# Performance work log

Hardware: AMD Instinct MI355X
Metric: run time of the kernel (lower is better)

## Reference

```python
import jax, jax.numpy as jnp
import numpy as np

B, S, C, H, W = 8, 32, 3, 256, 256


def setup_inputs() -> dict:
    key = jax.random.key(0)
    k1, k2 = jax.random.split(key)
    return {
        "input": jax.random.normal(k1, (B, S, C, H, W), dtype=jnp.float32),
        "target": jax.random.normal(k2, (B, C, H, W), dtype=jnp.float32),
    }


def _l2norm(x, axis):
    # F.normalize: x / max(||x||_2, eps)
    return x / jnp.maximum(jnp.linalg.norm(x, axis=axis, keepdims=True), 1e-12)


def _forward(input, target):
    b, s, c, h, w = input.shape
    # target: [B,C,H,W] -> permute(0,1,3,2) -> [B,C,W,H] -> flatten(1,2) -> [B, C*W, H]
    target_f = _l2norm(jnp.transpose(target, (0, 1, 3, 2)).reshape(b, c * w, h), axis=1)
    # input: [B,S,C,H,W] -> permute(0,1,2,4,3) -> [B,S,C,W,H] -> flatten(2,3) -> [B,S,C*W,H]
    input_f = _l2norm(jnp.transpose(input, (0, 1, 2, 4, 3)).reshape(b, s, c * w, h), axis=2)

    def corr_one(xf, wf):
        # xf: [S, C*W, H] as conv batch, wf: [C*W, H] as single-output-channel kernel
        y = jax.lax.conv_general_dilated(
            xf, wf[None], window_strides=(1,), padding=[(h - 1, h - 1)],
            dimension_numbers=("NCH", "OIH", "NCH"))
        return y[:, 0, :h]  # first H shift positions (overlap sizes 1..H)

    corr = jax.vmap(corr_one)(input_f, target_f)  # [B, S, H]
    corr = corr / jnp.arange(1, h + 1, dtype=input.dtype)  # mean over overlap size

    overlap = jnp.argmax(corr, axis=-1)            # [B, S] best overlap per sample
    shift = (h - 1) - overlap                      # rows to shift up by

    # out[b,s,:,r,:] = input[b,s,:,r+shift,:] for r < overlap, else 0
    h_idx = jnp.arange(h)[None, None, :] + shift[:, :, None]  # [B, S, H]
    valid = h_idx < h
    idx = jnp.clip(h_idx, 0, h - 1)[:, :, None, :, None]      # [B,S,1,H,1]
    gathered = jnp.take_along_axis(input, idx, axis=3)
    return jnp.where(valid[:, :, None, :, None], gathered, jnp.zeros((), input.dtype))


def reference(input, target):
    return _forward(input, target)
```

## Files before the change

### kernel.cpp

```cpp
#include <hip/hip_runtime.h>

#define B_ 8
#define S_ 32
#define C_ 3
#define H_ 256
#define W_ 256
#define HW_ (H_*W_)
#define CHW_ (C_*H_*W_)

typedef __attribute__((ext_vector_type(8))) short bf16x8;
typedef __attribute__((ext_vector_type(4))) float f32x4;

__device__ __forceinline__ void split2(float x, float y, unsigned &hp, unsigned &lp) {
  unsigned ux = __float_as_uint(x), uy = __float_as_uint(y);
  unsigned hx = ux & 0xFFFF0000u, hy = uy & 0xFFFF0000u;
  float lx = x - __uint_as_float(hx);
  float ly = y - __uint_as_float(hy);
  hp = (ux >> 16) | hy;
  lp = (__float_as_uint(lx) >> 16) | (__float_as_uint(ly) & 0xFFFF0000u);
}

__global__ __launch_bounds__(512)
void ct_corr_mfma(const float* __restrict__ input,
                  const float* __restrict__ target,
                  int* __restrict__ shift_out) {
  __shared__ ushort Ah[2][8192], Al[2][8192], Bh[2][8192], Bl[2][8192];
  __shared__ float ninSq[256], ntgSq[256], rnin[256], rntg[256], corrS[256];
  __shared__ unsigned long long wkey[4];

  const int bs = blockIdx.x;
  const int b  = bs >> 5;
  const int t  = threadIdx.x;
  const int lane = t & 63;
  const int wid  = t >> 6;
  const int wm   = wid >> 2;
  const int wn   = wid & 3;

  const float* Abase = input  + (size_t)bs * CHW_;
  const float* Tbase = target + (size_t)b  * CHW_;

  if (t < 256) { ninSq[t] = 0.f; ntgSq[t] = 0.f; corrS[t] = 0.f; }

  f32x4 acc[8][4];
#pragma unroll
  for (int m = 0; m < 8; ++m)
#pragma unroll
    for (int n = 0; n < 4; ++n) acc[m][n] = (f32x4){0.f, 0.f, 0.f, 0.f};

  float4 pa[4], pb[4];
  float ssA[4] = {0.f, 0.f, 0.f, 0.f};
  float ssB[4] = {0.f, 0.f, 0.f, 0.f};

  auto issue = [&](int kt) {
    const float* Ab = Abase + (size_t)(kt >> 3) * HW_ + (kt & 7) * 32;
    const float* Tb = Tbase + (size_t)(kt >> 3) * HW_ + (kt & 7) * 32;
#pragma unroll
    for (int p = 0; p < 4; ++p) {
      int f   = p * 512 + t;
      int row = (f >> 7) * 16 + ((f >> 1) & 15);
      int kk  = ((f >> 5) & 3) * 8 + (f & 1) * 4;
      pa[p] = *(const float4*)(Ab + (size_t)row * W_ + kk);
      pb[p] = *(const float4*)(Tb + (size_t)row * W_ + kk);
    }
  };

  auto stash = [&](int sel) {
    ushort* AhD = Ah[sel]; ushort* AlD = Al[sel];
    ushort* BhD = Bh[sel]; ushort* BlD = Bl[sel];
#pragma unroll
    for (int p = 0; p < 4; ++p) {
      int f   = p * 512 + t;
      int idx = (f >> 7) * 512 + ((f >> 5) & 3) * 128 + ((f >> 1) & 15) * 8 + (f & 1) * 4;
      float4 va = pa[p], vb = pb[p];
      ssA[p] = fmaf(va.x, va.x, fmaf(va.y, va.y, fmaf(va.z, va.z, fmaf(va.w, va.w, ssA[p]))));
      ssB[p] = fmaf(vb.x, vb.x, fmaf(vb.y, vb.y, fmaf(vb.z, vb.z, fmaf(vb.w, vb.w, ssB[p]))));
      unsigned h0, l0, h1, l1;
      split2(va.x, va.y, h0, l0); split2(va.z, va.w, h1, l1);
      *(uint2*)&AhD[idx] = make_uint2(h0, h1);
      *(uint2*)&AlD[idx] = make_uint2(l0, l1);
      split2(vb.x, vb.y, h0, l0); split2(vb.z, vb.w, h1, l1);
      *(uint2*)&BhD[idx] = make_uint2(h0, h1);
      *(uint2*)&BlD[idx] = make_uint2(l0, l1);
    }
  };

  issue(0);
  stash(0);
  issue(1);
  __syncthreads();

  for (int kt = 0; kt < 24; ++kt) {
    const int cur = kt & 1, nx = cur ^ 1;
    const ushort* AhC = Ah[cur]; const ushort* AlC = Al[cur];
    const ushort* BhC = Bh[cur]; const ushort* BlC = Bl[cur];

    bf16x8 bh[4], bl[4];
#pragma unroll
    for (int n = 0; n < 4; ++n) {
      int ct = wn * 4 + n;
      bh[n] = *(const bf16x8*)&BhC[ct * 512 + lane * 8];
      bl[n] = *(const bf16x8*)&BlC[ct * 512 + lane * 8];
    }
#pragma unroll
    for (int m = 0; m < 8; ++m) {
      int rt = wm * 8 + m;
      bf16x8 ah = *(const bf16x8*)&AhC[rt * 512 + lane * 8];
      bf16x8 al = *(const bf16x8*)&AlC[rt * 512 + lane * 8];
#pragma unroll
      for (int n = 0; n < 4; ++n) {
        acc[m][n] = __builtin_amdgcn_mfma_f32_16x16x32_bf16(ah, bh[n], acc[m][n], 0, 0, 0);
        acc[m][n] = __builtin_amdgcn_mfma_f32_16x16x32_bf16(ah, bl[n], acc[m][n], 0, 0, 0);
        acc[m][n] = __builtin_amdgcn_mfma_f32_16x16x32_bf16(al, bh[n], acc[m][n], 0, 0, 0);
      }
    }
    if (kt < 23) stash(nx);
    if (kt < 22) issue(kt + 2);
    __syncthreads();
  }

#pragma unroll
  for (int p = 0; p < 4; ++p) {
    int row = (p * 4 + (t >> 7)) * 16 + ((t >> 1) & 15);
    atomicAdd(&ninSq[row], ssA[p]);
    atomicAdd(&ntgSq[row], ssB[p]);
  }
  __syncthreads();
  if (t < 256) {
    rnin[t] = 1.0f / fmaxf(sqrtf(ninSq[t]), 1e-12f);
    rntg[t] = 1.0f / fmaxf(sqrtf(ntgSq[t]), 1e-12f);
  }
  __syncthreads();

#pragma unroll
  for (int n = 0; n < 4; ++n) {
    int col = wn * 64 + n * 16 + (lane & 15);
    float rc = rntg[col];
#pragma unroll
    for (int m = 0; m < 8; ++m) {
      f32x4 a = acc[m][n];
#pragma unroll
      for (int r = 0; r < 4; ++r) {
        int row = wm * 128 + m * 16 + (lane >> 4) * 4 + r;
        int q = col - row;
        if (q >= 0) atomicAdd(&corrS[q], a[r] * rnin[row] * rc);
      }
    }
  }
  __syncthreads();

  if (t < 256) {
    int q = 255 - t;
    float v = corrS[q] / (float)(256 - q);
    unsigned u = __float_as_uint(v);
    u = (u & 0x80000000u) ? ~u : (u | 0x80000000u);
    unsigned long long key = ((unsigned long long)u << 32) | (unsigned)q;
#pragma unroll
    for (int off = 32; off; off >>= 1) {
      unsigned long long o = __shfl_xor(key, off);
      if (o > key) key = o;
    }
    if ((t & 63) == 0) wkey[t >> 6] = key;
  }
  __syncthreads();
  if (t == 0) {
    unsigned long long k = wkey[0];
#pragma unroll
    for (int i = 1; i < 4; ++i) if (wkey[i] > k) k = wkey[i];
    shift_out[bs] = (int)(k & 0xFFFFFFFFull);
  }
}

__global__ void ct_gather(const float* __restrict__ input,
                          const int* __restrict__ shift,
                          float* __restrict__ out) {
  size_t idx = (size_t)blockIdx.x * blockDim.x + threadIdx.x;
  int w4 = (int)(idx & 63);
  int h  = (int)((idx >> 6) & 255);
  int sc = (int)(idx >> 14);
  int bs = sc / 3;
  int hh = h + shift[bs];
  float4 v = make_float4(0.f, 0.f, 0.f, 0.f);
  if (hh < H_) v = *(const float4*)(input + ((size_t)sc << 16) + (size_t)hh * W_ + w4*4);
  *(float4*)(out + (idx << 2)) = v;
}

extern "C" void kernel_launch(void* const* d_in, const int* in_sizes, int n_in,
                              void* d_out, int out_size, void* d_ws, size_t ws_size,
                              hipStream_t stream) {
  const float* input  = (const float*)d_in[0];
  const float* target = (const float*)d_in[1];
  float* out  = (float*)d_out;
  int*  shift = (int*)d_ws;

  ct_corr_mfma <<<B_ * S_, 512, 0, stream>>>(input, target, shift);
  ct_gather    <<<(B_*S_*C_*H_*W_/4) / 256, 256, 0, stream>>>(input, shift, out);
}
```

Measured before the change: 167.4 us.

## Pre-split target into bf16 hi/lo tiles and stream via direct global-to-LDS loads

```diff
diff --git a/kernel.cpp b/kernel.cpp
--- a/kernel.cpp
+++ b/kernel.cpp
@@ -7,9 +7,14 @@
 #define W_ 256
 #define HW_ (H_*W_)
 #define CHW_ (C_*H_*W_)
+#define NT_ 24
+#define TILE_ELEMS 8192
 
 typedef __attribute__((ext_vector_type(8))) short bf16x8;
 typedef __attribute__((ext_vector_type(4))) float f32x4;
+typedef unsigned int u32;
+typedef u32 __attribute__((address_space(3)))* lds_u32p;
+typedef const u32 __attribute__((address_space(1)))* glb_u32p;
 
 __device__ __forceinline__ void split2(float x, float y, unsigned &hp, unsigned &lp) {
   unsigned ux = __float_as_uint(x), uy = __float_as_uint(y);
@@ -20,26 +25,70 @@
   lp = (__float_as_uint(lx) >> 16) | (__float_as_uint(ly) & 0xFFFF0000u);
 }
 
+__device__ __forceinline__ void gl2lds16(const ushort* g, ushort* l) {
+  __builtin_amdgcn_global_load_lds((glb_u32p)g, (lds_u32p)l, 16, 0, 0);
+}
+
+__global__ void ct_ntg(const float* __restrict__ target, float* __restrict__ rntg) {
+  int r = (int)((blockIdx.x * (size_t)blockDim.x + threadIdx.x) >> 6);
+  int lane = threadIdx.x & 63;
+  const float* base = target + (size_t)(r >> 8) * CHW_ + (size_t)(r & 255) * W_;
+  float ss = 0.f;
+#pragma unroll
+  for (int c = 0; c < C_; ++c)
+#pragma unroll
+    for (int tt = 0; tt < W_/64; ++tt) {
+      float v = base[c*HW_ + tt*64 + lane];
+      ss = fmaf(v, v, ss);
+    }
+#pragma unroll
+  for (int off = 32; off; off >>= 1) ss += __shfl_xor(ss, off);
+  if (lane == 0) rntg[r] = 1.0f / fmaxf(sqrtf(ss), 1e-12f);
+}
+
+__global__ void ct_bsplit(const float* __restrict__ target,
+                          ushort* __restrict__ BhG, ushort* __restrict__ BlG) {
+  int bx = blockIdx.x;
+  int b  = bx / 24, kt = bx % 24;
+  int c  = kt >> 3, w0 = (kt & 7) * 32;
+  int t  = threadIdx.x;
+  int trow = t >> 3, tw = t & 7;
+  const float* base = target + (size_t)(b*C_ + c) * HW_ + w0 + tw*4;
+  ushort* oh = BhG + (size_t)bx * TILE_ELEMS;
+  ushort* ol = BlG + (size_t)bx * TILE_ELEMS;
+#pragma unroll
+  for (int i = 0; i < 8; ++i) {
+    int row = trow + 32*i;
+    float4 v = *(const float4*)(base + (size_t)row * W_);
+    unsigned h0, l0, h1, l1;
+    split2(v.x, v.y, h0, l0); split2(v.z, v.w, h1, l1);
+    int idx = (row>>4)*512 + (tw>>1)*128 + (row&15)*8 + (tw&1)*4;
+    *(uint2*)&oh[idx] = make_uint2(h0, h1);
+    *(uint2*)&ol[idx] = make_uint2(l0, l1);
+  }
+}
+
 __global__ __launch_bounds__(512)
 void ct_corr_mfma(const float* __restrict__ input,
-                  const float* __restrict__ target,
+                  const ushort* __restrict__ BhG, const ushort* __restrict__ BlG,
+                  const float* __restrict__ rntg_g,
                   int* __restrict__ shift_out) {
-  __shared__ ushort Ah[2][8192], Al[2][8192], Bh[2][8192], Bl[2][8192];
-  __shared__ float ninSq[256], ntgSq[256], rnin[256], rntg[256], corrS[256];
+  __shared__ ushort AhL[2][TILE_ELEMS], AlL[2][TILE_ELEMS];
+  __shared__ ushort BhL[2][TILE_ELEMS], BlL[2][TILE_ELEMS];
+  __shared__ float ninSq[256], rnin[256], rntg_s[256], corrS[256];
   __shared__ unsigned long long wkey[4];
 
   const int bs = blockIdx.x;
-  const int b  = bs >> 5;
+  const int bG = bs >> 5;
   const int t  = threadIdx.x;
   const int lane = t & 63;
   const int wid  = t >> 6;
   const int wm   = wid >> 2;
   const int wn   = wid & 3;
 
-  const float* Abase = input  + (size_t)bs * CHW_;
-  const float* Tbase = target + (size_t)b  * CHW_;
-
-  if (t < 256) { ninSq[t] = 0.f; ntgSq[t] = 0.f; corrS[t] = 0.f; }
+  const float* Abase = input + (size_t)bs * CHW_;
+
+  if (t < 256) { ninSq[t] = 0.f; corrS[t] = 0.f; rntg_s[t] = rntg_g[bG*256 + t]; }
 
   f32x4 acc[8][4];
 #pragma unroll
@@ -47,100 +96,127 @@
 #pragma unroll
     for (int n = 0; n < 4; ++n) acc[m][n] = (f32x4){0.f, 0.f, 0.f, 0.f};
 
-  float4 pa[4], pb[4];
+  float4 paE[4], paO[4];
   float ssA[4] = {0.f, 0.f, 0.f, 0.f};
-  float ssB[4] = {0.f, 0.f, 0.f, 0.f};
-
-  auto issue = [&](int kt) {
-    const float* Ab = Abase + (size_t)(kt >> 3) * HW_ + (kt & 7) * 32;
-    const float* Tb = Tbase + (size_t)(kt >> 3) * HW_ + (kt & 7) * 32;
-#pragma unroll
-    for (int p = 0; p < 4; ++p) {
-      int f   = p * 512 + t;
-      int row = (f >> 7) * 16 + ((f >> 1) & 15);
-      int kk  = ((f >> 5) & 3) * 8 + (f & 1) * 4;
-      pa[p] = *(const float4*)(Ab + (size_t)row * W_ + kk);
-      pb[p] = *(const float4*)(Tb + (size_t)row * W_ + kk);
-    }
-  };
-
-  auto stash = [&](int sel) {
-    ushort* AhD = Ah[sel]; ushort* AlD = Al[sel];
-    ushort* BhD = Bh[sel]; ushort* BlD = Bl[sel];
-#pragma unroll
-    for (int p = 0; p < 4; ++p) {
-      int f   = p * 512 + t;
-      int idx = (f >> 7) * 512 + ((f >> 5) & 3) * 128 + ((f >> 1) & 15) * 8 + (f & 1) * 4;
-      float4 va = pa[p], vb = pb[p];
-      ssA[p] = fmaf(va.x, va.x, fmaf(va.y, va.y, fmaf(va.z, va.z, fmaf(va.w, va.w, ssA[p]))));
-      ssB[p] = fmaf(vb.x, vb.x, fmaf(vb.y, vb.y, fmaf(vb.z, vb.z, fmaf(vb.w, vb.w, ssB[p]))));
-      unsigned h0, l0, h1, l1;
-      split2(va.x, va.y, h0, l0); split2(va.z, va.w, h1, l1);
-      *(uint2*)&AhD[idx] = make_uint2(h0, h1);
-      *(uint2*)&AlD[idx] = make_uint2(l0, l1);
-      split2(vb.x, vb.y, h0, l0); split2(vb.z, vb.w, h1, l1);
-      *(uint2*)&BhD[idx] = make_uint2(h0, h1);
-      *(uint2*)&BlD[idx] = make_uint2(l0, l1);
-    }
-  };
-
-  issue(0);
-  stash(0);
-  issue(1);
-  __syncthreads();
-
-  for (int kt = 0; kt < 24; ++kt) {
-    const int cur = kt & 1, nx = cur ^ 1;
-    const ushort* AhC = Ah[cur]; const ushort* AlC = Al[cur];
-    const ushort* BhC = Bh[cur]; const ushort* BlC = Bl[cur];
-
-    bf16x8 bh[4], bl[4];
-#pragma unroll
-    for (int n = 0; n < 4; ++n) {
-      int ct = wn * 4 + n;
-      bh[n] = *(const bf16x8*)&BhC[ct * 512 + lane * 8];
-      bl[n] = *(const bf16x8*)&BlC[ct * 512 + lane * 8];
-    }
-#pragma unroll
-    for (int m = 0; m < 8; ++m) {
-      int rt = wm * 8 + m;
-      bf16x8 ah = *(const bf16x8*)&AhC[rt * 512 + lane * 8];
-      bf16x8 al = *(const bf16x8*)&AlC[rt * 512 + lane * 8];
-#pragma unroll
-      for (int n = 0; n < 4; ++n) {
-        acc[m][n] = __builtin_amdgcn_mfma_f32_16x16x32_bf16(ah, bh[n], acc[m][n], 0, 0, 0);
-        acc[m][n] = __builtin_amdgcn_mfma_f32_16x16x32_bf16(ah, bl[n], acc[m][n], 0, 0, 0);
-        acc[m][n] = __builtin_amdgcn_mfma_f32_16x16x32_bf16(al, bh[n], acc[m][n], 0, 0, 0);
-      }
-    }
-    if (kt < 23) stash(nx);
-    if (kt < 22) issue(kt + 2);
-    __syncthreads();
-  }
+
+#define ISSUE_A(KT, PA) {                                                     \
+    const float* Ab = Abase + (size_t)((KT) >> 3) * HW_ + ((KT) & 7) * 32;    \
+    _Pragma("unroll")                                                         \
+    for (int p = 0; p < 4; ++p) {                                             \
+      int f = p*512 + t;                                                      \
+      int row = (f >> 7) * 16 + ((f >> 1) & 15);                              \
+      int kk  = ((f >> 5) & 3) * 8 + (f & 1) * 4;                             \
+      PA[p] = *(const float4*)(Ab + (size_t)row * W_ + kk);                   \
+    } }
+
+#define ISSUE_B(KT, NXP) {                                                    \
+    const ushort* gh = BhG + (size_t)(bG*NT_ + (KT)) * TILE_ELEMS + wn*2048;  \
+    const ushort* gl = BlG + (size_t)(bG*NT_ + (KT)) * TILE_ELEMS + wn*2048;  \
+    _Pragma("unroll")                                                         \
+    for (int o = 0; o < 4; ++o)                                               \
+      gl2lds16(gh + o*512 + lane*8, &BhL[NXP][wn*2048 + o*512]);              \
+    _Pragma("unroll")                                                         \
+    for (int o = 0; o < 4; ++o)                                               \
+      gl2lds16(gl + o*512 + lane*8, &BlL[NXP][wn*2048 + o*512]);              \
+    __builtin_amdgcn_sched_barrier(0); }
+
+#define STASH_A(PA, NXP) {                                                    \
+    _Pragma("unroll")                                                         \
+    for (int p = 0; p < 4; ++p) {                                             \
+      int f = p*512 + t;                                                      \
+      int idx = (f>>7)*512 + ((f>>5)&3)*128 + ((f>>1)&15)*8 + (f&1)*4;        \
+      float4 va = PA[p];                                                      \
+      ssA[p] = fmaf(va.x, va.x, fmaf(va.y, va.y,                              \
+               fmaf(va.z, va.z, fmaf(va.w, va.w, ssA[p]))));                  \
+      unsigned h0, l0, h1, l1;                                                \
+      split2(va.x, va.y, h0, l0); split2(va.z, va.w, h1, l1);                 \
+      *(uint2*)&AhL[NXP][idx] = make_uint2(h0, h1);                           \
+      *(uint2*)&AlL[NXP][idx] = make_uint2(l0, l1);                           \
+    } }
+
+#define MFMA_BODY(CURP) {                                                     \
+    bf16x8 bh[4], bl[4];                                                      \
+    _Pragma("unroll")                                                         \
+    for (int n = 0; n < 4; ++n) {                                             \
+      int ct = wn*4 + n;                                                      \
+      bh[n] = *(const bf16x8*)&BhL[CURP][ct*512 + lane*8];                    \
+      bl[n] = *(const bf16x8*)&BlL[CURP][ct*512 + lane*8];                    \
+    }                                                                         \
+    __builtin_amdgcn_s_setprio(1);                                            \
+    _Pragma("unroll")                                                         \
+    for (int m = 0; m < 8; ++m) {                                             \
+      int rt = wm*8 + m;                                                      \
+      bf16x8 ah = *(const bf16x8*)&AhL[CURP][rt*512 + lane*8];                \
+      bf16x8 al = *(const bf16x8*)&AlL[CURP][rt*512 + lane*8];                \
+      _Pragma("unroll")                                                       \
+      for (int n = 0; n < 4; ++n) {                                           \
+        acc[m][n] = __builtin_amdgcn_mfma_f32_16x16x32_bf16(ah, bh[n], acc[m][n], 0, 0, 0); \
+        acc[m][n] = __builtin_amdgcn_mfma_f32_16x16x32_bf16(ah, bl[n], acc[m][n], 0, 0, 0); \
+        acc[m][n] = __builtin_amdgcn_mfma_f32_16x16x32_bf16(al, bh[n], acc[m][n], 0, 0, 0); \
+      }                                                                       \
+    }                                                                         \
+    __builtin_amdgcn_s_setprio(0); }
+
+#define WAIT_VM4() { asm volatile("s_waitcnt vmcnt(4)" ::: "memory");         \
+                     __builtin_amdgcn_sched_barrier(0); }
+#define WAIT_VM0() { asm volatile("s_waitcnt vmcnt(0)" ::: "memory");         \
+                     __builtin_amdgcn_sched_barrier(0); }
+#define BAR() { asm volatile("s_waitcnt lgkmcnt(0)" ::: "memory");            \
+                __builtin_amdgcn_sched_barrier(0);                            \
+                __builtin_amdgcn_s_barrier();                                 \
+                __builtin_amdgcn_sched_barrier(0); }
+
+  ISSUE_A(0, paE);
+  __builtin_amdgcn_sched_barrier(0);
+  ISSUE_B(0, 0);
+  ISSUE_A(1, paO);
+  __builtin_amdgcn_sched_barrier(0);
+  STASH_A(paE, 0);
+  BAR();
+
+#define TILE_EVEN(KT, DO_A) {                                                 \
+    WAIT_VM4();                                                               \
+    ISSUE_B((KT)+1, 1);                                                       \
+    MFMA_BODY(0);                                                             \
+    STASH_A(paO, 1);                                                          \
+    if (DO_A) { ISSUE_A((KT)+2, paE); }                                       \
+    BAR(); }
+#define TILE_ODD(KT) {                                                        \
+    WAIT_VM4();                                                               \
+    ISSUE_B((KT)+1, 0);                                                       \
+    MFMA_BODY(1);                                                             \
+    STASH_A(paE, 0);                                                          \
+    ISSUE_A((KT)+2, paO);                                                     \
+    BAR(); }
+
+  for (int it = 0; it < 11; ++it) {
+    int k0 = 2*it;
+    TILE_EVEN(k0, true);
+    TILE_ODD(k0 + 1);
+  }
+  TILE_EVEN(22, false);
+  WAIT_VM0();
+  MFMA_BODY(1);
 
 #pragma unroll
   for (int p = 0; p < 4; ++p) {
-    int row = (p * 4 + (t >> 7)) * 16 + ((t >> 1) & 15);
+    int row = (p*4 + (t >> 7)) * 16 + ((t >> 1) & 15);
     atomicAdd(&ninSq[row], ssA[p]);
-    atomicAdd(&ntgSq[row], ssB[p]);
-  }
-  __syncthreads();
-  if (t < 256) {
-    rnin[t] = 1.0f / fmaxf(sqrtf(ninSq[t]), 1e-12f);
-    rntg[t] = 1.0f / fmaxf(sqrtf(ntgSq[t]), 1e-12f);
-  }
+  }
+  __syncthreads();
+  if (t < 256) rnin[t] = 1.0f / fmaxf(sqrtf(ninSq[t]), 1e-12f);
   __syncthreads();
 
 #pragma unroll
   for (int n = 0; n < 4; ++n) {
-    int col = wn * 64 + n * 16 + (lane & 15);
-    float rc = rntg[col];
+    int col = wn*64 + n*16 + (lane & 15);
+    float rc = rntg_s[col];
 #pragma unroll
     for (int m = 0; m < 8; ++m) {
       f32x4 a = acc[m][n];
 #pragma unroll
       for (int r = 0; r < 4; ++r) {
-        int row = wm * 128 + m * 16 + (lane >> 4) * 4 + r;
+        int row = wm*128 + m*16 + (lane >> 4)*4 + r;
         int q = col - row;
         if (q >= 0) atomicAdd(&corrS[q], a[r] * rnin[row] * rc);
       }
@@ -189,9 +265,15 @@
                               hipStream_t stream) {
   const float* input  = (const float*)d_in[0];
   const float* target = (const float*)d_in[1];
-  float* out  = (float*)d_out;
-  int*  shift = (int*)d_ws;
-
-  ct_corr_mfma <<<B_ * S_, 512, 0, stream>>>(input, target, shift);
+  float* out = (float*)d_out;
+
+  float* rntg = (float*)d_ws;
+  int* shift  = (int*)(rntg + 2048);
+  ushort* BhG = (ushort*)(shift + 256);
+  ushort* BlG = BhG + (size_t)B_ * NT_ * TILE_ELEMS;
+
+  ct_ntg       <<<512, 256, 0, stream>>>(target, rntg);
+  ct_bsplit    <<<B_ * NT_, 256, 0, stream>>>(target, BhG, BlG);
+  ct_corr_mfma <<<B_ * S_, 512, 0, stream>>>(input, BhG, BlG, rntg, shift);
   ct_gather    <<<(B_*S_*C_*H_*W_/4) / 256, 256, 0, stream>>>(input, shift, out);
 }
```

Result: slower. 172.5 us (+3.0%).
